# Optimization experiments

Measured on AMD Instinct MI355X. Metric: run time of the kernel, lower is better.

Reference implementation:

```python
import jax, jax.numpy as jnp
import numpy as np
import math

B, T, N, D = 2, 2048, 16, 128


def setup_inputs() -> dict:
    key = jax.random.key(0)
    ks = jax.random.split(key, 9)
    s = 1.0 / math.sqrt(D)
    return {
        "x": jax.random.normal(ks[0], (B, T, N, D), dtype=jnp.float32),
        "wq": jax.random.normal(ks[1], (D, D), dtype=jnp.float32) * s,
        "bq": jax.random.normal(ks[2], (D,), dtype=jnp.float32) * 0.02,
        "wk": jax.random.normal(ks[3], (D, D), dtype=jnp.float32) * s,
        "bk": jax.random.normal(ks[4], (D,), dtype=jnp.float32) * 0.02,
        "wv": jax.random.normal(ks[5], (D, D), dtype=jnp.float32) * s,
        "bv": jax.random.normal(ks[6], (D,), dtype=jnp.float32) * 0.02,
        "wp": jax.random.normal(ks[7], (D, D), dtype=jnp.float32) * s,
        "bp": jax.random.normal(ks[8], (D,), dtype=jnp.float32) * 0.02,
    }


def reference(x, wq, bq, wk, bk, wv, bv, wp, bp):
    # x: (B, T, N, D); per-head Linear projections (torch y = x @ W.T + b)
    d = x.shape[-1]
    q = jnp.einsum("btnd,ed->btne", x, wq) + bq  # (B,T,N,D)
    k = jnp.einsum("btnd,ed->btne", x, wk) + bk
    v = jnp.einsum("btnd,ed->btne", x, wv) + bv
    scale = 1.0 / jnp.sqrt(jnp.asarray(d, dtype=x.dtype))
    # scores: (B, N, T, T)
    scores = jnp.einsum("btnd,bsnd->bnts", q, k) * scale
    t = scores.shape[-1]
    causal = jnp.tril(jnp.ones((t, t), dtype=bool))  # (T,T)
    scores = jnp.where(causal[None, None], scores, jnp.asarray(-jnp.inf, scores.dtype))
    w = jax.nn.softmax(scores, axis=-1)
    att = jnp.einsum("bnts,bsnd->btnd", w, v)  # (B,T,N,D)
    out = jnp.einsum("btnd,ed->btne", att, wp) + bp
    return out
```

## Files before the change

### kernel.cpp

```cpp
#include <hip/hip_runtime.h>
#include <cmath>

#define BB 2
#define TT 2048
#define NN 16
#define DD 128
#define NROWS (BB*TT*NN)
#define PLANE (TT*DD)
#define KP 132
#define VP 68
#define TP 129

typedef unsigned short u16;
typedef unsigned int   u32;
typedef __attribute__((ext_vector_type(8)))  short s8v;
typedef __attribute__((ext_vector_type(16))) float vf16;

__device__ u16 g_Q [(size_t)NROWS * DD];
__device__ u16 g_K [(size_t)NROWS * DD];
__device__ u16 g_VT[(size_t)NROWS * DD];

__device__ __forceinline__ u16 f2bf(float f) {
    return (u16)((__float_as_uint(f) + 0x8000u) >> 16);
}
__device__ __forceinline__ u32 pk2(float a, float b) {
    return ((__float_as_uint(a) + 0x8000u) >> 16)
         | ((__float_as_uint(b) + 0x8000u) & 0xFFFF0000u);
}
__device__ __forceinline__ void st8(u16* p, const float4& a, const float4& b) {
    uint2 lo, hi;
    lo.x = pk2(a.x, a.y); lo.y = pk2(a.z, a.w);
    hi.x = pk2(b.x, b.y); hi.y = pk2(b.z, b.w);
    *(uint2*)p       = lo;
    *(uint2*)(p + 4) = hi;
}
__device__ __forceinline__ s8v ld8(const u16* p) {
    short4 a = *(const short4*)p;
    short4 b = *(const short4*)(p + 4);
    return (s8v){a.x, a.y, a.z, a.w, b.x, b.y, b.z, b.w};
}

__device__ __forceinline__ void bar_lds()
{
    asm volatile("s_waitcnt lgkmcnt(0)" ::: "memory");
    __builtin_amdgcn_sched_barrier(0);
    __builtin_amdgcn_s_barrier();
    __builtin_amdgcn_sched_barrier(0);
}

__global__ __launch_bounds__(256)
void qkv_proj_kernel(const float* __restrict__ x,
                     const float* __restrict__ Wq, const float* __restrict__ Bq,
                     const float* __restrict__ Wk, const float* __restrict__ Bk,
                     const float* __restrict__ Wv, const float* __restrict__ Bv)
{
    __shared__ u16 Xs[128*KP];
    __shared__ u16 Ws[128*KP];

    const int t    = threadIdx.x;
    const int bnp  = blockIdx.x >> 4;
    const int tt0  = (blockIdx.x & 15) * 128;
    const size_t xrow0 = ((size_t)((bnp >> 4)*TT + tt0)*NN + (bnp & 15)) * DD;

    #pragma unroll
    for (int it = 0; it < 8; ++it) {
        int i = t + 256*it;
        int e = i >> 4, c8 = i & 15;
        const float* xp = x + xrow0 + (size_t)e*(NN*DD) + c8*8;
        st8(&Xs[e*KP + c8*8], *(const float4*)xp, *(const float4*)(xp + 4));
    }
    #pragma unroll
    for (int it = 0; it < 8; ++it) {
        int i = t + 256*it;
        int e = i >> 4, c8 = i & 15;
        st8(&Ws[e*KP + c8*8], ((const float4*)Wq)[2*i], ((const float4*)Wq)[2*i + 1]);
    }
    __syncthreads();

    const int w   = t >> 6;
    const int l31 = t & 31;
    const int q2  = (t >> 5) & 1;

    s8v af[8];
    #pragma unroll
    for (int s = 0; s < 8; ++s)
        af[s] = ld8(&Xs[(w*32 + l31)*KP + s*16 + q2*8]);

    #pragma unroll
    for (int wsel = 0; wsel < 3; ++wsel) {
        const float* Bi = (wsel == 0) ? Bq : (wsel == 1) ? Bk : Bv;

        vf16 acc[4];
        #pragma unroll
        for (int et = 0; et < 4; ++et)
            #pragma unroll
            for (int i = 0; i < 16; ++i) acc[et][i] = 0.f;

        #pragma unroll
        for (int s = 0; s < 8; ++s) {
            #pragma unroll
            for (int et = 0; et < 4; ++et) {
                s8v bf = ld8(&Ws[(et*32 + l31)*KP + s*16 + q2*8]);
                acc[et] = __builtin_amdgcn_mfma_f32_32x32x16_bf16(af[s], bf, acc[et], 0, 0, 0);
            }
        }

        float bb[4];
        #pragma unroll
        for (int et = 0; et < 4; ++et) bb[et] = Bi[et*32 + l31];

        if (wsel < 2) {
            u16* Ot = (wsel == 0) ? g_Q : g_K;
            #pragma unroll
            for (int r = 0; r < 16; ++r) {
                int rl = (r & 3) + 8*(r >> 2) + 4*q2;
                size_t orow = (size_t)bnp*PLANE + (size_t)(tt0 + w*32 + rl)*DD;
                #pragma unroll
                for (int et = 0; et < 4; ++et) {
                    float ov = acc[et][r] + bb[et];
                    if (wsel == 0) ov *= 0.12752053685940512f;
                    Ot[orow + et*32 + l31] = f2bf(ov);
                }
            }
            const float* Wn = (wsel == 0) ? Wk : Wv;
            __syncthreads();
            #pragma unroll
            for (int it = 0; it < 8; ++it) {
                int i = t + 256*it;
                int e = i >> 4, c8 = i & 15;
                st8(&Ws[e*KP + c8*8], ((const float4*)Wn)[2*i], ((const float4*)Wn)[2*i + 1]);
            }
            __syncthreads();
        } else {
            u16* Xt = (u16*)Xs;
            #pragma unroll
            for (int r = 0; r < 16; ++r) {
                int rl = (r & 3) + 8*(r >> 2) + 4*q2;
                int row = w*32 + rl;
                #pragma unroll
                for (int et = 0; et < 4; ++et)
                    Xt[row*TP + et*32 + l31] = f2bf(acc[et][r] + bb[et]);
            }
            __syncthreads();
            const size_t vbase = (size_t)bnp*PLANE + tt0;
            #pragma unroll
            for (int c = 0; c < 8; ++c) {
                int idx = t + 256*c;
                int d = idx >> 4, tc = idx & 15;
                u16 e8[8];
                #pragma unroll
                for (int i = 0; i < 8; ++i) e8[i] = Xt[(tc*8 + i)*TP + d];
                uint4 pkv;
                pkv.x = (u32)e8[0] | ((u32)e8[1] << 16);
                pkv.y = (u32)e8[2] | ((u32)e8[3] << 16);
                pkv.z = (u32)e8[4] | ((u32)e8[5] << 16);
                pkv.w = (u32)e8[6] | ((u32)e8[7] << 16);
                *(uint4*)&g_VT[vbase + (size_t)d*TT + tc*8] = pkv;
            }
        }
    }
}

__global__ __launch_bounds__(256, 2)
void attn_kernel(const float* __restrict__ Wp, const float* __restrict__ Bp,
                 float* __restrict__ out)
{
    __shared__ u16 Ks[2][64*KP];
    __shared__ u16 Vt[2][128*VP];

    const int t   = threadIdx.x;
    const int grp = blockIdx.x >> 5;
    const int bn  = blockIdx.x & 31;
    const int qt  = (grp < 8) ? (15 - grp) : (grp - 8);
    const int q0  = qt * 128;
    const size_t plane = (size_t)bn * PLANE;
    const u16* Kg = g_K  + plane;
    const u16* Vg = g_VT + plane;

    const int w      = t >> 6;
    const int lane   = t & 63;
    const int lane31 = lane & 31;
    const int q2     = lane >> 5;
    const int qband  = q0 + 32*w;
    const int qrow   = qband + lane31;

    s8v qf[8];
    {
        const u16* Qg = g_Q + plane + (size_t)qrow * DD;
        #pragma unroll
        for (int s = 0; s < 8; ++s)
            qf[s] = *(const s8v*)&Qg[s*16 + q2*8];
    }

    vf16 accO[4];
    #pragma unroll
    for (int dt = 0; dt < 4; ++dt)
        #pragma unroll
        for (int i = 0; i < 16; ++i) accO[dt][i] = 0.f;

    float lrow = 0.f;
    const int nkt = 2*qt + 2;

    uint4 pk[4], pv[4];

    auto LOADT = [&](int kt) {
        const u16* K2 = Kg + (size_t)(kt*64)*DD;
        const u16* V2 = Vg + kt*64;
        #pragma unroll
        for (int c = 0; c < 4; ++c) {
            int j = t + 256*c;
            int kr = j >> 4, kc = j & 15;
            pk[c] = *(const uint4*)&K2[kr*DD + kc*8];
            int vr = j >> 3, vc = j & 7;
            pv[c] = *(const uint4*)&V2[(size_t)vr*TT + vc*8];
        }
    };
    auto STORET = [&](int buf) {
        #pragma unroll
        for (int c = 0; c < 4; ++c) {
            int j = t + 256*c;
            int kr = j >> 4, kc = j & 15;
            uint2 a, b;
            a.x = pk[c].x; a.y = pk[c].y; b.x = pk[c].z; b.y = pk[c].w;
            *(uint2*)&Ks[buf][kr*KP + kc*8]     = a;
            *(uint2*)&Ks[buf][kr*KP + kc*8 + 4] = b;
            int vr = j >> 3, vc = j & 7;
            a.x = pv[c].x; a.y = pv[c].y; b.x = pv[c].z; b.y = pv[c].w;
            *(uint2*)&Vt[buf][vr*VP + vc*8]     = a;
            *(uint2*)&Vt[buf][vr*VP + vc*8 + 4] = b;
        }
    };

    LOADT(0);
    STORET(0);
    LOADT(1);

    for (int kt = 0; kt < nkt; ++kt) {
        const int k0 = kt*64;
        const int cb = kt & 1;
        bar_lds();

        if (kt + 1 < nkt) {
            STORET(cb ^ 1);
            if (kt + 2 < nkt) LOADT(kt + 2);
        }

        if (k0 <= qband + 31) {
            const u16* Kb = Ks[cb];
            const u16* Vb = Vt[cb];

            vf16 accS[2];
            #pragma unroll
            for (int kk = 0; kk < 2; ++kk)
                #pragma unroll
                for (int i = 0; i < 16; ++i) accS[kk][i] = 0.f;
            __builtin_amdgcn_s_setprio(1);
            #pragma unroll
            for (int s = 0; s < 8; ++s) {
                #pragma unroll
                for (int kk = 0; kk < 2; ++kk) {
                    s8v a = ld8(&Kb[(kk*32 + lane31)*KP + s*16 + q2*8]);
                    accS[kk] = __builtin_amdgcn_mfma_f32_32x32x16_bf16(a, qf[s], accS[kk], 0, 0, 0);
                }
            }
            __builtin_amdgcn_s_setprio(0);

            float p[2][16];
            const bool tail = (k0 + 63 > qband);
            #pragma unroll
            for (int kk = 0; kk < 2; ++kk)
                #pragma unroll
                for (int r = 0; r < 16; ++r) {
                    float sv = accS[kk][r];
                    if (tail) {
                        int keyg = k0 + kk*32 + (r & 3) + 8*(r >> 2) + 4*q2;
                        if (keyg > qrow) sv = -INFINITY;
                    }
                    p[kk][r] = sv;
                }

            float ls0 = 0.f, ls1 = 0.f;
            #pragma unroll
            for (int r = 0; r < 16; ++r) {
                float e0 = __builtin_amdgcn_exp2f(p[0][r] - 16.f);
                float e1 = __builtin_amdgcn_exp2f(p[1][r] - 16.f);
                p[0][r] = e0; p[1][r] = e1;
                ls0 += e0; ls1 += e1;
            }
            float ls = ls0 + ls1;
            ls += __shfl_xor(ls, 32);
            lrow += ls;

            s8v pf[4];
            #pragma unroll
            for (int tau = 0; tau < 4; ++tau) {
                int kk = tau >> 1, rb = (tau & 1)*8;
                s8v v;
                #pragma unroll
                for (int j = 0; j < 8; ++j)
                    v[j] = (short)(__float_as_uint(p[kk][rb + j]) >> 16);
                pf[tau] = v;
            }

            __builtin_amdgcn_s_setprio(1);
            #pragma unroll
            for (int dt = 0; dt < 4; ++dt) {
                const u16* vp = &Vb[(dt*32 + lane31)*VP];
                #pragma unroll
                for (int tau = 0; tau < 4; ++tau) {
                    const u16* q = vp + 16*tau + 4*q2;
                    short4 lo = *(const short4*)q;
                    short4 hi = *(const short4*)(q + 8);
                    s8v bvv = {lo.x, lo.y, lo.z, lo.w, hi.x, hi.y, hi.z, hi.w};
                    accO[dt] = __builtin_amdgcn_mfma_f32_32x32x16_bf16(pf[tau], bvv, accO[dt], 0, 0, 0);
                }
            }
            __builtin_amdgcn_s_setprio(0);
        }
    }

    bar_lds();
    u16* Os  = &Ks[0][0];
    u16* Wps = &Vt[0][0];

    {
        float inv = 1.0f / lrow;
        #pragma unroll
        for (int r = 0; r < 16; ++r) {
            int rl = (r & 3) + 8*(r >> 2) + 4*q2;
            float ir = __shfl(inv, rl);
            u16* op = &Os[(32*w + rl)*KP];
            #pragma unroll
            for (int dt = 0; dt < 4; ++dt)
                op[dt*32 + lane31] = f2bf(accO[dt][r] * ir);
        }
    }
    #pragma unroll
    for (int it = 0; it < 8; ++it) {
        int i = t + 256*it;
        int e = i >> 4, c8 = i & 15;
        st8(&Wps[e*KP + c8*8], ((const float4*)Wp)[2*i], ((const float4*)Wp)[2*i + 1]);
    }
    bar_lds();

    {
        s8v af[8];
        #pragma unroll
        for (int s = 0; s < 8; ++s)
            af[s] = ld8(&Os[(w*32 + lane31)*KP + s*16 + q2*8]);

        vf16 acc[4];
        #pragma unroll
        for (int et = 0; et < 4; ++et)
            #pragma unroll
            for (int i = 0; i < 16; ++i) acc[et][i] = 0.f;

        #pragma unroll
        for (int s = 0; s < 8; ++s) {
            #pragma unroll
            for (int et = 0; et < 4; ++et) {
                s8v bf = ld8(&Wps[(et*32 + lane31)*KP + s*16 + q2*8]);
                acc[et] = __builtin_amdgcn_mfma_f32_32x32x16_bf16(af[s], bf, acc[et], 0, 0, 0);
            }
        }

        float bb[4];
        #pragma unroll
        for (int et = 0; et < 4; ++et) bb[et] = Bp[et*32 + lane31];

        const int b = bn >> 4, n = bn & 15;
        #pragma unroll
        for (int r = 0; r < 16; ++r) {
            int rl = (r & 3) + 8*(r >> 2) + 4*q2;
            int qg = q0 + w*32 + rl;
            size_t orow = ((size_t)(b*TT + qg)*NN + n) * DD;
            #pragma unroll
            for (int et = 0; et < 4; ++et)
                out[orow + et*32 + lane31] = acc[et][r] + bb[et];
        }
    }
}

extern "C" void kernel_launch(void* const* d_in, const int* in_sizes, int n_in,
                              void* d_out, int out_size, void* d_ws, size_t ws_size,
                              hipStream_t stream)
{
    const float* x  = (const float*)d_in[0];
    const float* wq = (const float*)d_in[1];
    const float* bq = (const float*)d_in[2];
    const float* wk = (const float*)d_in[3];
    const float* bk = (const float*)d_in[4];
    const float* wv = (const float*)d_in[5];
    const float* bv = (const float*)d_in[6];
    const float* wp = (const float*)d_in[7];
    const float* bp = (const float*)d_in[8];
    float* out = (float*)d_out;
    (void)d_ws; (void)ws_size;

    qkv_proj_kernel<<<dim3(NROWS/128), dim3(256), 0, stream>>>(
        x, wq, bq, wk, bk, wv, bv);
    attn_kernel<<<dim3(BB*NN*(TT/128)), dim3(256), 0, stream>>>(wp, bp, out);
}
```

Baseline: 172.5 us.

## Stage K/V via direct global-to-LDS loads and split keys across wave pairs

Replaces register-staged K/V tile loads with global_load_lds direct-to-LDS transfers using XOR-swizzled layouts, and permutes the V-transpose write in the projection kernel to match the MFMA fragment order. Work is restructured so each wave handles 64 query rows and half of each 64-key tile. Every K fragment read from LDS is now reused for two MFMAs, and each V fragment serves two query subtiles. The partial O accumulators and row sums from the two key-halves are reduced through LDS at the end. This costs more registers, which may hurt occupancy under launch_bounds(256,2), plus an extra LDS reduction and a full vmcnt wait every iteration.

```diff
diff --git a/kernel.cpp b/kernel.cpp
--- a/kernel.cpp
+++ b/kernel.cpp
@@ -8,7 +8,6 @@
 #define NROWS (BB*TT*NN)
 #define PLANE (TT*DD)
 #define KP 132
-#define VP 68
 #define TP 129
 
 typedef unsigned short u16;
@@ -47,6 +46,19 @@
     __builtin_amdgcn_s_barrier();
     __builtin_amdgcn_sched_barrier(0);
 }
+__device__ __forceinline__ void bar_vm()
+{
+    asm volatile("s_waitcnt vmcnt(0) lgkmcnt(0)" ::: "memory");
+    __builtin_amdgcn_sched_barrier(0);
+    __builtin_amdgcn_s_barrier();
+    __builtin_amdgcn_sched_barrier(0);
+}
+__device__ __forceinline__ void gl_lds(const u16* g, u16* l)
+{
+    __builtin_amdgcn_global_load_lds(
+        (const __attribute__((address_space(1))) void*)g,
+        (__attribute__((address_space(3))) void*)l, 16, 0, 0);
+}
 
 __global__ __launch_bounds__(256)
 void qkv_proj_kernel(const float* __restrict__ x,
@@ -146,16 +158,18 @@
             #pragma unroll
             for (int c = 0; c < 8; ++c) {
                 int idx = t + 256*c;
-                int d = idx >> 4, tc = idx & 15;
+                int d = idx >> 4, pc = idx & 15;
+                int G = pc >> 1, h = pc & 1;
                 u16 e8[8];
                 #pragma unroll
-                for (int i = 0; i < 8; ++i) e8[i] = Xt[(tc*8 + i)*TP + d];
+                for (int i = 0; i < 8; ++i)
+                    e8[i] = Xt[(G*16 + h*4 + (i & 3) + 8*(i >> 2))*TP + d];
                 uint4 pkv;
                 pkv.x = (u32)e8[0] | ((u32)e8[1] << 16);
                 pkv.y = (u32)e8[2] | ((u32)e8[3] << 16);
                 pkv.z = (u32)e8[4] | ((u32)e8[5] << 16);
                 pkv.w = (u32)e8[6] | ((u32)e8[7] << 16);
-                *(uint4*)&g_VT[vbase + (size_t)d*TT + tc*8] = pkv;
+                *(uint4*)&g_VT[vbase + (size_t)d*TT + pc*8] = pkv;
             }
         }
     }
@@ -165,8 +179,7 @@
 void attn_kernel(const float* __restrict__ Wp, const float* __restrict__ Bp,
                  float* __restrict__ out)
 {
-    __shared__ u16 Ks[2][64*KP];
-    __shared__ u16 Vt[2][128*VP];
+    __shared__ __align__(16) u16 S[33792];
 
     const int t   = threadIdx.x;
     const int grp = blockIdx.x >> 5;
@@ -177,164 +190,178 @@
     const u16* Kg = g_K  + plane;
     const u16* Vg = g_VT + plane;
 
-    const int w      = t >> 6;
-    const int lane   = t & 63;
-    const int lane31 = lane & 31;
-    const int q2     = lane >> 5;
-    const int qband  = q0 + 32*w;
-    const int qrow   = qband + lane31;
-
-    s8v qf[8];
-    {
-        const u16* Qg = g_Q + plane + (size_t)qrow * DD;
+    const int w    = t >> 6;
+    const int lane = t & 63;
+    const int l31  = lane & 31;
+    const int q2   = lane >> 5;
+    const int qb   = (w >> 1) * 64;
+    const int kh   = (w & 1) * 32;
+
+    s8v qf[2][8];
+    #pragma unroll
+    for (int qs = 0; qs < 2; ++qs) {
+        const u16* Qg = g_Q + plane + (size_t)(q0 + qb + qs*32 + l31) * DD;
         #pragma unroll
         for (int s = 0; s < 8; ++s)
-            qf[s] = *(const s8v*)&Qg[s*16 + q2*8];
-    }
-
-    vf16 accO[4];
-    #pragma unroll
-    for (int dt = 0; dt < 4; ++dt)
-        #pragma unroll
-        for (int i = 0; i < 16; ++i) accO[dt][i] = 0.f;
-
-    float lrow = 0.f;
+            qf[qs][s] = *(const s8v*)&Qg[s*16 + q2*8];
+    }
+
+    vf16 accO[2][4];
+    #pragma unroll
+    for (int qs = 0; qs < 2; ++qs)
+        #pragma unroll
+        for (int dt = 0; dt < 4; ++dt)
+            #pragma unroll
+            for (int i = 0; i < 16; ++i) accO[qs][dt][i] = 0.f;
+
+    float lrow[2] = {0.f, 0.f};
     const int nkt = 2*qt + 2;
 
-    uint4 pk[4], pv[4];
-
-    auto LOADT = [&](int kt) {
-        const u16* K2 = Kg + (size_t)(kt*64)*DD;
-        const u16* V2 = Vg + kt*64;
-        #pragma unroll
-        for (int c = 0; c < 4; ++c) {
-            int j = t + 256*c;
-            int kr = j >> 4, kc = j & 15;
-            pk[c] = *(const uint4*)&K2[kr*DD + kc*8];
-            int vr = j >> 3, vc = j & 7;
-            pv[c] = *(const uint4*)&V2[(size_t)vr*TT + vc*8];
+    auto STAGE = [&](int kt, int buf) {
+        const int w4 = w*4;
+        #pragma unroll
+        for (int i = 0; i < 4; ++i) {
+            int ch = w4 + i;
+            int r  = ch*4 + (lane >> 4);
+            int sl = (lane & 15) ^ (r & 15);
+            gl_lds(Kg + (size_t)(kt*64 + r)*DD + sl*8,
+                   &S[buf*8192 + ch*512]);
+        }
+        #pragma unroll
+        for (int i = 0; i < 4; ++i) {
+            int ch = w4 + i;
+            int d  = ch*8 + (lane >> 3);
+            int sl = (lane & 7) ^ ((d ^ (d >> 3)) & 7);
+            gl_lds(Vg + (size_t)d*TT + kt*64 + sl*8,
+                   &S[16384 + buf*8192 + ch*512]);
         }
     };
-    auto STORET = [&](int buf) {
-        #pragma unroll
-        for (int c = 0; c < 4; ++c) {
-            int j = t + 256*c;
-            int kr = j >> 4, kc = j & 15;
-            uint2 a, b;
-            a.x = pk[c].x; a.y = pk[c].y; b.x = pk[c].z; b.y = pk[c].w;
-            *(uint2*)&Ks[buf][kr*KP + kc*8]     = a;
-            *(uint2*)&Ks[buf][kr*KP + kc*8 + 4] = b;
-            int vr = j >> 3, vc = j & 7;
-            a.x = pv[c].x; a.y = pv[c].y; b.x = pv[c].z; b.y = pv[c].w;
-            *(uint2*)&Vt[buf][vr*VP + vc*8]     = a;
-            *(uint2*)&Vt[buf][vr*VP + vc*8 + 4] = b;
-        }
-    };
-
-    LOADT(0);
-    STORET(0);
-    LOADT(1);
-
+
+    STAGE(0, 0);
     for (int kt = 0; kt < nkt; ++kt) {
+        const int cb = kt & 1;
+        bar_vm();
+        if (kt + 1 < nkt) STAGE(kt + 1, cb ^ 1);
+
         const int k0 = kt*64;
-        const int cb = kt & 1;
-        bar_lds();
-
-        if (kt + 1 < nkt) {
-            STORET(cb ^ 1);
-            if (kt + 2 < nkt) LOADT(kt + 2);
-        }
-
-        if (k0 <= qband + 31) {
-            const u16* Kb = Ks[cb];
-            const u16* Vb = Vt[cb];
+        if (k0 + kh <= q0 + qb + 63) {
+            const u16* Kb = &S[cb*8192];
+            const u16* Vb = &S[16384 + cb*8192];
 
             vf16 accS[2];
             #pragma unroll
-            for (int kk = 0; kk < 2; ++kk)
-                #pragma unroll
-                for (int i = 0; i < 16; ++i) accS[kk][i] = 0.f;
+            for (int qs = 0; qs < 2; ++qs)
+                #pragma unroll
+                for (int i = 0; i < 16; ++i) accS[qs][i] = 0.f;
             __builtin_amdgcn_s_setprio(1);
             #pragma unroll
             for (int s = 0; s < 8; ++s) {
-                #pragma unroll
-                for (int kk = 0; kk < 2; ++kk) {
-                    s8v a = ld8(&Kb[(kk*32 + lane31)*KP + s*16 + q2*8]);
-                    accS[kk] = __builtin_amdgcn_mfma_f32_32x32x16_bf16(a, qf[s], accS[kk], 0, 0, 0);
-                }
+                int r  = kh + l31;
+                int sl = (2*s + q2) ^ (r & 15);
+                s8v a = *(const s8v*)&Kb[r*128 + sl*8];
+                accS[0] = __builtin_amdgcn_mfma_f32_32x32x16_bf16(a, qf[0][s], accS[0], 0, 0, 0);
+                accS[1] = __builtin_amdgcn_mfma_f32_32x32x16_bf16(a, qf[1][s], accS[1], 0, 0, 0);
             }
             __builtin_amdgcn_s_setprio(0);
 
-            float p[2][16];
-            const bool tail = (k0 + 63 > qband);
-            #pragma unroll
-            for (int kk = 0; kk < 2; ++kk)
+            #pragma unroll
+            for (int qs = 0; qs < 2; ++qs) {
+                const bool tail = (k0 + kh + 31) > (q0 + qb + qs*32);
+                float ls = 0.f;
                 #pragma unroll
                 for (int r = 0; r < 16; ++r) {
-                    float sv = accS[kk][r];
+                    float sv = accS[qs][r];
                     if (tail) {
-                        int keyg = k0 + kk*32 + (r & 3) + 8*(r >> 2) + 4*q2;
+                        int keyg = k0 + kh + (r & 3) + 8*(r >> 2) + 4*q2;
+                        int qrow = q0 + qb + qs*32 + l31;
                         if (keyg > qrow) sv = -INFINITY;
                     }
-                    p[kk][r] = sv;
+                    float e = __builtin_amdgcn_exp2f(sv - 16.f);
+                    accS[qs][r] = e;
+                    ls += e;
                 }
-
-            float ls0 = 0.f, ls1 = 0.f;
+                ls += __shfl_xor(ls, 32);
+                lrow[qs] += ls;
+            }
+
+            __builtin_amdgcn_s_setprio(1);
+            #pragma unroll
+            for (int tau = 0; tau < 2; ++tau) {
+                s8v pf0, pf1;
+                #pragma unroll
+                for (int j = 0; j < 8; ++j) {
+                    pf0[j] = (short)(__float_as_uint(accS[0][tau*8 + j]) >> 16);
+                    pf1[j] = (short)(__float_as_uint(accS[1][tau*8 + j]) >> 16);
+                }
+                #pragma unroll
+                for (int dt = 0; dt < 4; ++dt) {
+                    int d  = dt*32 + l31;
+                    int sl = ((kh >> 3) + 2*tau + q2) ^ ((d ^ (d >> 3)) & 7);
+                    s8v bv = *(const s8v*)&Vb[d*64 + sl*8];
+                    accO[0][dt] = __builtin_amdgcn_mfma_f32_32x32x16_bf16(pf0, bv, accO[0][dt], 0, 0, 0);
+                    accO[1][dt] = __builtin_amdgcn_mfma_f32_32x32x16_bf16(pf1, bv, accO[1][dt], 0, 0, 0);
+                }
+            }
+            __builtin_amdgcn_s_setprio(0);
+        }
+    }
+
+    bar_lds();
+    float* Cf = (float*)S;
+    float* LF = (float*)(S + 32768);
+    if (kh) {
+        float* dst = Cf + (qb >> 6)*8192;
+        #pragma unroll
+        for (int qs = 0; qs < 2; ++qs)
+            #pragma unroll
+            for (int dt = 0; dt < 4; ++dt) {
+                float* p4 = dst + (qs*4 + dt)*1024 + lane*16;
+                #pragma unroll
+                for (int k = 0; k < 4; ++k)
+                    *(float4*)&p4[k*4] = make_float4(accO[qs][dt][4*k],   accO[qs][dt][4*k+1],
+                                                     accO[qs][dt][4*k+2], accO[qs][dt][4*k+3]);
+            }
+        LF[qb + l31]      = lrow[0];
+        LF[qb + 32 + l31] = lrow[1];
+    }
+    bar_lds();
+    u16* OsP = S;
+    if (!kh) {
+        const float* src = Cf + (qb >> 6)*8192;
+        #pragma unroll
+        for (int qs = 0; qs < 2; ++qs)
+            #pragma unroll
+            for (int dt = 0; dt < 4; ++dt) {
+                const float* p4 = src + (qs*4 + dt)*1024 + lane*16;
+                #pragma unroll
+                for (int k = 0; k < 4; ++k) {
+                    float4 v = *(const float4*)&p4[k*4];
+                    accO[qs][dt][4*k]   += v.x;
+                    accO[qs][dt][4*k+1] += v.y;
+                    accO[qs][dt][4*k+2] += v.z;
+                    accO[qs][dt][4*k+3] += v.w;
+                }
+            }
+        lrow[0] += LF[qb + l31];
+        lrow[1] += LF[qb + 32 + l31];
+    }
+    bar_lds();
+    if (!kh) {
+        #pragma unroll
+        for (int qs = 0; qs < 2; ++qs) {
+            float iv = 1.0f / lrow[qs];
             #pragma unroll
             for (int r = 0; r < 16; ++r) {
-                float e0 = __builtin_amdgcn_exp2f(p[0][r] - 16.f);
-                float e1 = __builtin_amdgcn_exp2f(p[1][r] - 16.f);
-                p[0][r] = e0; p[1][r] = e1;
-                ls0 += e0; ls1 += e1;
-            }
-            float ls = ls0 + ls1;
-            ls += __shfl_xor(ls, 32);
-            lrow += ls;
-
-            s8v pf[4];
-            #pragma unroll
-            for (int tau = 0; tau < 4; ++tau) {
-                int kk = tau >> 1, rb = (tau & 1)*8;
-                s8v v;
-                #pragma unroll
-                for (int j = 0; j < 8; ++j)
-                    v[j] = (short)(__float_as_uint(p[kk][rb + j]) >> 16);
-                pf[tau] = v;
-            }
-
-            __builtin_amdgcn_s_setprio(1);
-            #pragma unroll
-            for (int dt = 0; dt < 4; ++dt) {
-                const u16* vp = &Vb[(dt*32 + lane31)*VP];
-                #pragma unroll
-                for (int tau = 0; tau < 4; ++tau) {
-                    const u16* q = vp + 16*tau + 4*q2;
-                    short4 lo = *(const short4*)q;
-                    short4 hi = *(const short4*)(q + 8);
-                    s8v bvv = {lo.x, lo.y, lo.z, lo.w, hi.x, hi.y, hi.z, hi.w};
-                    accO[dt] = __builtin_amdgcn_mfma_f32_32x32x16_bf16(pf[tau], bvv, accO[dt], 0, 0, 0);
-                }
-            }
-            __builtin_amdgcn_s_setprio(0);
-        }
-    }
-
-    bar_lds();
-    u16* Os  = &Ks[0][0];
-    u16* Wps = &Vt[0][0];
-
-    {
-        float inv = 1.0f / lrow;
-        #pragma unroll
-        for (int r = 0; r < 16; ++r) {
-            int rl = (r & 3) + 8*(r >> 2) + 4*q2;
-            float ir = __shfl(inv, rl);
-            u16* op = &Os[(32*w + rl)*KP];
-            #pragma unroll
-            for (int dt = 0; dt < 4; ++dt)
-                op[dt*32 + lane31] = f2bf(accO[dt][r] * ir);
-        }
-    }
+                int rl = (r & 3) + 8*(r >> 2) + 4*q2;
+                float ir = __shfl(iv, rl);
+                u16* op = &OsP[(qb + qs*32 + rl)*KP];
+                #pragma unroll
+                for (int dt = 0; dt < 4; ++dt)
+                    op[dt*32 + l31] = f2bf(accO[qs][dt][r] * ir);
+            }
+        }
+    }
+    u16* Wps = S + 16896;
     #pragma unroll
     for (int it = 0; it < 8; ++it) {
         int i = t + 256*it;
@@ -347,7 +374,7 @@
         s8v af[8];
         #pragma unroll
         for (int s = 0; s < 8; ++s)
-            af[s] = ld8(&Os[(w*32 + lane31)*KP + s*16 + q2*8]);
+            af[s] = ld8(&OsP[(w*32 + l31)*KP + s*16 + q2*8]);
 
         vf16 acc[4];
         #pragma unroll
@@ -359,14 +386,14 @@
         for (int s = 0; s < 8; ++s) {
             #pragma unroll
             for (int et = 0; et < 4; ++et) {
-                s8v bf = ld8(&Wps[(et*32 + lane31)*KP + s*16 + q2*8]);
+                s8v bf = ld8(&Wps[(et*32 + l31)*KP + s*16 + q2*8]);
                 acc[et] = __builtin_amdgcn_mfma_f32_32x32x16_bf16(af[s], bf, acc[et], 0, 0, 0);
             }
         }
 
         float bb[4];
         #pragma unroll
-        for (int et = 0; et < 4; ++et) bb[et] = Bp[et*32 + lane31];
+        for (int et = 0; et < 4; ++et) bb[et] = Bp[et*32 + l31];
 
         const int b = bn >> 4, n = bn & 15;
         #pragma unroll
@@ -376,7 +403,7 @@
             size_t orow = ((size_t)(b*TT + qg)*NN + n) * DD;
             #pragma unroll
             for (int et = 0; et < 4; ++et)
-                out[orow + et*32 + lane31] = acc[et][r] + bb[et];
+                out[orow + et*32 + l31] = acc[et][r] + bb[et];
         }
     }
 }
```

Result: slower. 223.3 us (+29.4%).

## Swizzle K/V shared-memory tiles and pre-permute V^T for 128-bit LDS reads

Applied to the files above, without the earlier changes.

Replaces the padded K and V^T shared tiles with unpadded XOR-swizzled layouts, so the fragments feeding the QK and PV MFMAs come from single 128-bit LDS loads and stores instead of split 64-bit ones. The V-transpose stage of the projection kernel now writes V^T with keys permuted into MFMA accumulator order, so each P-fragment's eight keys sit contiguously and the PV operand loads need no regathering. This is meant to cut LDS instruction count and bank conflicts in the attention inner loop. It depends on the swizzle and permutation staying consistent across both kernels, and it reshuffles the epilogue's shared-memory offsets.

```diff
diff --git a/kernel.cpp b/kernel.cpp
--- a/kernel.cpp
+++ b/kernel.cpp
@@ -8,7 +8,6 @@
 #define NROWS (BB*TT*NN)
 #define PLANE (TT*DD)
 #define KP 132
-#define VP 68
 #define TP 129
 
 typedef unsigned short u16;
@@ -146,16 +145,18 @@
             #pragma unroll
             for (int c = 0; c < 8; ++c) {
                 int idx = t + 256*c;
-                int d = idx >> 4, tc = idx & 15;
+                int d = idx >> 4, pc = idx & 15;
+                int G = pc >> 1, h = pc & 1;
                 u16 e8[8];
                 #pragma unroll
-                for (int i = 0; i < 8; ++i) e8[i] = Xt[(tc*8 + i)*TP + d];
+                for (int i = 0; i < 8; ++i)
+                    e8[i] = Xt[(G*16 + h*4 + (i & 3) + 8*(i >> 2))*TP + d];
                 uint4 pkv;
                 pkv.x = (u32)e8[0] | ((u32)e8[1] << 16);
                 pkv.y = (u32)e8[2] | ((u32)e8[3] << 16);
                 pkv.z = (u32)e8[4] | ((u32)e8[5] << 16);
                 pkv.w = (u32)e8[6] | ((u32)e8[7] << 16);
-                *(uint4*)&g_VT[vbase + (size_t)d*TT + tc*8] = pkv;
+                *(uint4*)&g_VT[vbase + (size_t)d*TT + pc*8] = pkv;
             }
         }
     }
@@ -165,8 +166,7 @@
 void attn_kernel(const float* __restrict__ Wp, const float* __restrict__ Bp,
                  float* __restrict__ out)
 {
-    __shared__ u16 Ks[2][64*KP];
-    __shared__ u16 Vt[2][128*VP];
+    __shared__ __align__(16) u16 S[33792];
 
     const int t   = threadIdx.x;
     const int grp = blockIdx.x >> 5;
@@ -179,10 +179,10 @@
 
     const int w      = t >> 6;
     const int lane   = t & 63;
-    const int lane31 = lane & 31;
+    const int l31    = lane & 31;
     const int q2     = lane >> 5;
     const int qband  = q0 + 32*w;
-    const int qrow   = qband + lane31;
+    const int qrow   = qband + l31;
 
     s8v qf[8];
     {
@@ -220,14 +220,11 @@
         for (int c = 0; c < 4; ++c) {
             int j = t + 256*c;
             int kr = j >> 4, kc = j & 15;
-            uint2 a, b;
-            a.x = pk[c].x; a.y = pk[c].y; b.x = pk[c].z; b.y = pk[c].w;
-            *(uint2*)&Ks[buf][kr*KP + kc*8]     = a;
-            *(uint2*)&Ks[buf][kr*KP + kc*8 + 4] = b;
+            int slk = kc ^ (kr & 15);
+            *(uint4*)&S[buf*8192 + kr*128 + slk*8] = pk[c];
             int vr = j >> 3, vc = j & 7;
-            a.x = pv[c].x; a.y = pv[c].y; b.x = pv[c].z; b.y = pv[c].w;
-            *(uint2*)&Vt[buf][vr*VP + vc*8]     = a;
-            *(uint2*)&Vt[buf][vr*VP + vc*8 + 4] = b;
+            int slv = vc ^ ((vr ^ (vr >> 3)) & 7);
+            *(uint4*)&S[16384 + buf*8192 + vr*64 + slv*8] = pv[c];
         }
     };
 
@@ -246,8 +243,8 @@
         }
 
         if (k0 <= qband + 31) {
-            const u16* Kb = Ks[cb];
-            const u16* Vb = Vt[cb];
+            const u16* Kb = &S[cb*8192];
+            const u16* Vb = &S[16384 + cb*8192];
 
             vf16 accS[2];
             #pragma unroll
@@ -259,7 +256,9 @@
             for (int s = 0; s < 8; ++s) {
                 #pragma unroll
                 for (int kk = 0; kk < 2; ++kk) {
-                    s8v a = ld8(&Kb[(kk*32 + lane31)*KP + s*16 + q2*8]);
+                    int r  = kk*32 + l31;
+                    int sl = (2*s + q2) ^ (r & 15);
+                    s8v a = *(const s8v*)&Kb[r*128 + sl*8];
                     accS[kk] = __builtin_amdgcn_mfma_f32_32x32x16_bf16(a, qf[s], accS[kk], 0, 0, 0);
                 }
             }
@@ -305,14 +304,14 @@
             __builtin_amdgcn_s_setprio(1);
             #pragma unroll
             for (int dt = 0; dt < 4; ++dt) {
-                const u16* vp = &Vb[(dt*32 + lane31)*VP];
+                int d = dt*32 + l31;
+                int fd = (d ^ (d >> 3)) & 7;
                 #pragma unroll
                 for (int tau = 0; tau < 4; ++tau) {
-                    const u16* q = vp + 16*tau + 4*q2;
-                    short4 lo = *(const short4*)q;
-                    short4 hi = *(const short4*)(q + 8);
-                    s8v bvv = {lo.x, lo.y, lo.z, lo.w, hi.x, hi.y, hi.z, hi.w};
-                    accO[dt] = __builtin_amdgcn_mfma_f32_32x32x16_bf16(pf[tau], bvv, accO[dt], 0, 0, 0);
+                    int c  = 4*(tau >> 1) + 2*(tau & 1) + q2;
+                    int sl = c ^ fd;
+                    s8v bv = *(const s8v*)&Vb[d*64 + sl*8];
+                    accO[dt] = __builtin_amdgcn_mfma_f32_32x32x16_bf16(pf[tau], bv, accO[dt], 0, 0, 0);
                 }
             }
             __builtin_amdgcn_s_setprio(0);
@@ -320,8 +319,8 @@
     }
 
     bar_lds();
-    u16* Os  = &Ks[0][0];
-    u16* Wps = &Vt[0][0];
+    u16* Os  = &S[0];
+    u16* Wps = &S[16896];
 
     {
         float inv = 1.0f / lrow;
@@ -332,7 +331,7 @@
             u16* op = &Os[(32*w + rl)*KP];
             #pragma unroll
             for (int dt = 0; dt < 4; ++dt)
-                op[dt*32 + lane31] = f2bf(accO[dt][r] * ir);
+                op[dt*32 + l31] = f2bf(accO[dt][r] * ir);
         }
     }
     #pragma unroll
@@ -347,7 +346,7 @@
         s8v af[8];
         #pragma unroll
         for (int s = 0; s < 8; ++s)
-            af[s] = ld8(&Os[(w*32 + lane31)*KP + s*16 + q2*8]);
+            af[s] = ld8(&Os[(w*32 + l31)*KP + s*16 + q2*8]);
 
         vf16 acc[4];
         #pragma unroll
@@ -359,14 +358,14 @@
         for (int s = 0; s < 8; ++s) {
             #pragma unroll
             for (int et = 0; et < 4; ++et) {
-                s8v bf = ld8(&Wps[(et*32 + lane31)*KP + s*16 + q2*8]);
+                s8v bf = ld8(&Wps[(et*32 + l31)*KP + s*16 + q2*8]);
                 acc[et] = __builtin_amdgcn_mfma_f32_32x32x16_bf16(af[s], bf, acc[et], 0, 0, 0);
             }
         }
 
         float bb[4];
         #pragma unroll
-        for (int et = 0; et < 4; ++et) bb[et] = Bp[et*32 + lane31];
+        for (int et = 0; et < 4; ++et) bb[et] = Bp[et*32 + l31];
 
         const int b = bn >> 4, n = bn & 15;
         #pragma unroll
@@ -376,7 +375,7 @@
             size_t orow = ((size_t)(b*TT + qg)*NN + n) * DD;
             #pragma unroll
             for (int et = 0; et < 4; ++et)
-                out[orow + et*32 + lane31] = acc[et][r] + bb[et];
+                out[orow + et*32 + l31] = acc[et][r] + bb[et];
         }
     }
 }
```

Result: slower. 223.1 us (+29.3%).
